# Performance work log

Measured on AMD Instinct MI355X. Metric: run time of the kernel, lower is better.

The kernel has to match this reference:

```python
import jax, jax.numpy as jnp
import numpy as np


def chamfer_l2(x, y):
    # x: [B,N1,3], y: [B,N2,3]; squared-L2 pairwise distances via Gram trick
    x2 = jnp.sum(x * x, axis=-1)                     # [B,N1]
    y2 = jnp.sum(y * y, axis=-1)                     # [B,N2]
    xy = jnp.einsum('bnd,bmd->bnm', x, y)            # [B,N1,N2]
    d = x2[:, :, None] + y2[:, None, :] - 2.0 * xy   # [B,N1,N2]
    cham_x = jnp.min(d, axis=2)                      # [B,N1] min over gt
    cham_y = jnp.min(d, axis=1)                      # [B,N2] min over pred
    return jnp.mean(cham_x) + jnp.mean(cham_y)


def setup_inputs() -> dict:
    key = jax.random.key(0)
    k1, k2, k3 = jax.random.split(key, 3)
    B = 4
    coarse_pc = jax.random.normal(k1, (B, 1024, 3), dtype=jnp.float32)
    fine_pc = jax.random.normal(k2, (B, 8192, 3), dtype=jnp.float32)
    gt_pc = jax.random.normal(k3, (B, 8192, 3), dtype=jnp.float32)
    return {"coarse_pc": coarse_pc, "fine_pc": fine_pc, "gt_pc": gt_pc,
            "param_coarse": 1000, "param_fine": 1000}


def reference(coarse_pc, fine_pc, gt_pc, param_coarse, param_fine):
    loss_coarse = chamfer_l2(coarse_pc, gt_pc) * param_coarse
    loss_fine = chamfer_l2(fine_pc, gt_pc) * param_fine
    return jnp.stack([loss_coarse, loss_fine])
```

## Files before the change

### kernel.cpp

```cpp
#include <hip/hip_runtime.h>

constexpr int NMINS = 102400;
constexpr int NBLK  = 2304;

typedef __attribute__((ext_vector_type(8)))  short bf16x8;
typedef __attribute__((ext_vector_type(16))) float f32x16;

__device__ __forceinline__ void split2(float v, unsigned& h, unsigned& l) {
    const unsigned uh = __float_as_uint(v) & 0xFFFF0000u;
    h = uh >> 16;
    l = __float_as_uint(v - __uint_as_float(uh)) >> 16;
}


__global__ __launch_bounds__(256, 3) void pccl_stage(
    const float* __restrict__ Xc, const float* __restrict__ Xf,
    const float* __restrict__ G, unsigned* __restrict__ mins,
    float* __restrict__ out)
{
    __shared__ uint4 alo[512];
    __shared__ uint4 ahi[512];
    const int tid  = threadIdx.x;
    const int lane = tid & 63;
    const int l31  = lane & 31;
    const bool hi  = lane >= 32;
    const int wv   = __builtin_amdgcn_readfirstlane(tid >> 6);
    const int W    = blockIdx.x;

    if (W == 0 && tid == 0) { out[0] = 0.0f; out[1] = 0.0f; }

    const float* Xp; const float* Yp;
    int NX, NY, ls, lc, local, mbase;
    if (W < 128)        { Xp=Xc; Yp=G;  NX=1024; NY=8192; ls=4; lc=1; local=W;      mbase=0; }
    else if (W < 256)   { Xp=G;  Yp=Xc; NX=8192; NY=1024; ls=1; lc=4; local=W-128;  mbase=4096; }
    else if (W < 1280)  { Xp=Xf; Yp=G;  NX=8192; NY=8192; ls=4; lc=4; local=W-256;  mbase=36864; }
    else                { Xp=G;  Yp=Xf; NX=8192; NY=8192; ls=4; lc=4; local=W-1280; mbase=69632; }
    const int split  = local & ((1 << ls) - 1);
    const int rest   = local >> ls;
    const int chunk4 = rest & ((1 << lc) - 1);
    const int b      = rest >> lc;

    const float* yg = Yp + ((size_t)b * NY + (size_t)split * 512) * 3;
    #pragma unroll
    for (int it = 0; it < 2; ++it) {
        const int pt = tid + 256 * it;
        const float y0 = yg[pt*3+0], y1 = yg[pt*3+1], y2 = yg[pt*3+2];
        const float w  = fmaf(y0, y0, fmaf(y1, y1, y2 * y2));
        unsigned h0, L0, h1, L1, h2, L2, hw, Lw;
        split2(y0, h0, L0); split2(y1, h1, L1);
        split2(y2, h2, L2); split2(w,  hw, Lw);
        alo[pt] = make_uint4(h0 | (L0 << 16), h0 | (h1 << 16),
                             L1 | (h1 << 16), h2 | (L2 << 16));
        ahi[pt] = make_uint4(h2 | (hw << 16), Lw, 0u, 0u);
    }

    const float* xg = Xp + ((size_t)b * NX + (size_t)chunk4 * 512 + (size_t)wv * 128) * 3;
    bf16x8 Bf[4]; float x2s[4];
    #pragma unroll
    for (int f = 0; f < 4; ++f) {
        const int p = f * 32 + l31;
        const float x0 = xg[p*3+0], x1 = xg[p*3+1], x2 = xg[p*3+2];
        x2s[f] = fmaf(x0, x0, fmaf(x1, x1, x2 * x2));
        unsigned sh0, sl0, sh1, sl1, sh2, sl2;
        split2(-2.f * x0, sh0, sl0);
        split2(-2.f * x1, sh1, sl1);
        split2(-2.f * x2, sh2, sl2);
        union { unsigned u[4]; bf16x8 v; } bu;
        bu.u[0] = hi ? (sl2 | (0x3F80u << 16)) : (sh0 | (sh0 << 16));
        bu.u[1] = hi ? 0x3F80u                 : (sl0 | (sh1 << 16));
        bu.u[2] = hi ? 0u                      : (sh1 | (sl1 << 16));
        bu.u[3] = hi ? 0u                      : (sh2 | (sh2 << 16));
        Bf[f] = bu.v;
    }

    float best[4][4];
    #pragma unroll
    for (int f = 0; f < 4; ++f)
        #pragma unroll
        for (int j = 0; j < 4; ++j) best[f][j] = 3.0e38f;

    const f32x16 zc = (f32x16)0.0f;
    const uint4* __restrict__ abase = hi ? ahi : alo;

    __syncthreads();

    #define FOLD(f, acc)                                                      \
        {                                                                     \
            _Pragma("unroll")                                                 \
            for (int j = 0; j < 4; ++j) {                                     \
                const float t3 = fminf(fminf((acc)[4*j], (acc)[4*j+1]),       \
                                       (acc)[4*j+2]);                         \
                best[f][j] = fminf(fminf(best[f][j], t3), (acc)[4*j+3]);      \
            }                                                                 \
        }

    uint4 dd = abase[l31];
    #pragma unroll 2
    for (int t = 0; t < 16; ++t) {
        union { uint4 u; bf16x8 v; } au; au.u = dd;
        const bf16x8 Af = au.v;
        const f32x16 a0 = __builtin_amdgcn_mfma_f32_32x32x16_bf16(Af, Bf[0], zc, 0, 0, 0);
        const f32x16 a1 = __builtin_amdgcn_mfma_f32_32x32x16_bf16(Af, Bf[1], zc, 0, 0, 0);
        const f32x16 a2 = __builtin_amdgcn_mfma_f32_32x32x16_bf16(Af, Bf[2], zc, 0, 0, 0);
        const f32x16 a3 = __builtin_amdgcn_mfma_f32_32x32x16_bf16(Af, Bf[3], zc, 0, 0, 0);
        dd = abase[(((t + 1) & 15) * 32) + l31];
        FOLD(0, a0);
        FOLD(1, a1);
        FOLD(2, a2);
        FOLD(3, a3);
    }
    #undef FOLD

    unsigned* mp = mins + mbase + b * NX + chunk4 * 512 + wv * 128;
    #pragma unroll
    for (int f = 0; f < 4; ++f) {
        float tm = fminf(fminf(best[f][0], best[f][1]),
                         fminf(best[f][2], best[f][3]));
        tm = fminf(tm, __shfl_xor(tm, 32, 64));
        const float d = fmaxf(x2s[f] + tm, 0.0f);
        atomicMin(mp + f * 32 + l31, __float_as_uint(d));
    }
}

__global__ __launch_bounds__(256) void pccl_sum(
    const unsigned* __restrict__ mins,
    const int* __restrict__ pc, const int* __restrict__ pf,
    float* __restrict__ out)
{
    const int tid  = threadIdx.x;
    const int lane = tid & 63;
    const int wv   = tid >> 6;
    const int q    = blockIdx.x * 256 + tid;
    const uint4 v  = ((const uint4*)mins)[q];
    float s = __uint_as_float(v.x) + __uint_as_float(v.y)
            + __uint_as_float(v.z) + __uint_as_float(v.w);
    #pragma unroll
    for (int off = 1; off < 64; off <<= 1) s += __shfl_xor(s, off, 64);
    __shared__ float sb[4];
    if (lane == 0) sb[wv] = s;
    __syncthreads();
    if (tid == 0) {
        const float t = sb[0] + sb[1] + sb[2] + sb[3];
        const int qb = blockIdx.x * 256;
        float w; int idx;
        if (qb < 1024)      { w = (1.f/4096.f)  * (float)pc[0]; idx = 0; }
        else if (qb < 9216) { w = (1.f/32768.f) * (float)pc[0]; idx = 0; }
        else                { w = (1.f/32768.f) * (float)pf[0]; idx = 1; }
        atomicAdd(out + idx, t * w);
    }
}

extern "C" void kernel_launch(void* const* d_in, const int* in_sizes, int n_in,
                              void* d_out, int out_size, void* d_ws, size_t ws_size,
                              hipStream_t stream) {
    const float* coarse = (const float*)d_in[0];
    const float* fine   = (const float*)d_in[1];
    const float* gt     = (const float*)d_in[2];
    const int*   pc     = (const int*)d_in[3];
    const int*   pf     = (const int*)d_in[4];
    float* out = (float*)d_out;
    unsigned* mins = (unsigned*)d_ws;

    pccl_stage<<<NBLK, 256, 0, stream>>>(coarse, fine, gt, mins, out);
    pccl_sum<<<100, 256, 0, stream>>>(mins, pc, pf, out);
}
```

Baseline: 81.99 us.

## Process three tiles per block with double-buffered LDS and prefetched loads

The grid shrinks to a third of its size, and each block now loops over three work tiles (block index plus multiples of the new grid size). While the MFMA loop runs on the current tile, the next tile's global loads are issued into registers. They are then packed into the other LDS buffer, and the previous tile's atomicMin stores are deferred so they overlap with later work. This hides global-load latency and per-block prologue cost. The price is higher register pressure under launch_bounds(256,3), double the LDS use, and fewer blocks to balance across CUs.

Measured after the change: 83.92 us. +2.4%, slower.

```diff
diff --git a/kernel.cpp b/kernel.cpp
--- a/kernel.cpp
+++ b/kernel.cpp
@@ -1,7 +1,7 @@
 #include <hip/hip_runtime.h>
 
 constexpr int NMINS = 102400;
-constexpr int NBLK  = 2304;
+constexpr int NBLK  = 768;
 
 typedef __attribute__((ext_vector_type(8)))  short bf16x8;
 typedef __attribute__((ext_vector_type(16))) float f32x16;
@@ -12,77 +12,89 @@
     l = __float_as_uint(v - __uint_as_float(uh)) >> 16;
 }
 
+__device__ __forceinline__ void packA(float y0, float y1, float y2,
+                                      uint4& lo, uint4& h4) {
+    const float w = fmaf(y0, y0, fmaf(y1, y1, y2 * y2));
+    unsigned h0, L0, h1, L1, h2, L2, hw, Lw;
+    split2(y0, h0, L0); split2(y1, h1, L1);
+    split2(y2, h2, L2); split2(w,  hw, Lw);
+    lo = make_uint4(h0 | (L0 << 16), h0 | (h1 << 16),
+                    L1 | (h1 << 16), h2 | (L2 << 16));
+    h4 = make_uint4(h2 | (hw << 16), Lw, 0u, 0u);
+}
+
+__device__ __forceinline__ bf16x8 packB(float x0, float x1, float x2, bool hi) {
+    unsigned sh0, sl0, sh1, sl1, sh2, sl2;
+    split2(-2.f * x0, sh0, sl0);
+    split2(-2.f * x1, sh1, sl1);
+    split2(-2.f * x2, sh2, sl2);
+    union { unsigned u[4]; bf16x8 v; } bu;
+    bu.u[0] = hi ? (sl2 | (0x3F80u << 16)) : (sh0 | (sh0 << 16));
+    bu.u[1] = hi ? 0x3F80u                 : (sl0 | (sh1 << 16));
+    bu.u[2] = hi ? 0u                      : (sh1 | (sl1 << 16));
+    bu.u[3] = hi ? 0u                      : (sh2 | (sh2 << 16));
+    return bu.v;
+}
+
+struct Geom { const float* Xp; const float* Yp; int NX, NY, mbase, split, chunk4, b; };
+
+__device__ __forceinline__ Geom decode(int W, const float* Xc,
+                                       const float* Xf, const float* G) {
+    Geom g; int ls, lc, local;
+    if (W < 128)        { g.Xp=Xc; g.Yp=G;  g.NX=1024; g.NY=8192; ls=4; lc=1; local=W;      g.mbase=0; }
+    else if (W < 256)   { g.Xp=G;  g.Yp=Xc; g.NX=8192; g.NY=1024; ls=1; lc=4; local=W-128;  g.mbase=4096; }
+    else if (W < 1280)  { g.Xp=Xf; g.Yp=G;  g.NX=8192; g.NY=8192; ls=4; lc=4; local=W-256;  g.mbase=36864; }
+    else                { g.Xp=G;  g.Yp=Xf; g.NX=8192; g.NY=8192; ls=4; lc=4; local=W-1280; g.mbase=69632; }
+    g.split  = local & ((1 << ls) - 1);
+    const int rest = local >> ls;
+    g.chunk4 = rest & ((1 << lc) - 1);
+    g.b      = rest >> lc;
+    return g;
+}
 
 __global__ __launch_bounds__(256, 3) void pccl_stage(
     const float* __restrict__ Xc, const float* __restrict__ Xf,
     const float* __restrict__ G, unsigned* __restrict__ mins,
     float* __restrict__ out)
 {
-    __shared__ uint4 alo[512];
-    __shared__ uint4 ahi[512];
+    __shared__ uint4 alo[2][512];
+    __shared__ uint4 ahi[2][512];
     const int tid  = threadIdx.x;
     const int lane = tid & 63;
     const int l31  = lane & 31;
     const bool hi  = lane >= 32;
     const int wv   = __builtin_amdgcn_readfirstlane(tid >> 6);
-    const int W    = blockIdx.x;
-
-    if (W == 0 && tid == 0) { out[0] = 0.0f; out[1] = 0.0f; }
-
-    const float* Xp; const float* Yp;
-    int NX, NY, ls, lc, local, mbase;
-    if (W < 128)        { Xp=Xc; Yp=G;  NX=1024; NY=8192; ls=4; lc=1; local=W;      mbase=0; }
-    else if (W < 256)   { Xp=G;  Yp=Xc; NX=8192; NY=1024; ls=1; lc=4; local=W-128;  mbase=4096; }
-    else if (W < 1280)  { Xp=Xf; Yp=G;  NX=8192; NY=8192; ls=4; lc=4; local=W-256;  mbase=36864; }
-    else                { Xp=G;  Yp=Xf; NX=8192; NY=8192; ls=4; lc=4; local=W-1280; mbase=69632; }
-    const int split  = local & ((1 << ls) - 1);
-    const int rest   = local >> ls;
-    const int chunk4 = rest & ((1 << lc) - 1);
-    const int b      = rest >> lc;
-
-    const float* yg = Yp + ((size_t)b * NY + (size_t)split * 512) * 3;
-    #pragma unroll
-    for (int it = 0; it < 2; ++it) {
-        const int pt = tid + 256 * it;
-        const float y0 = yg[pt*3+0], y1 = yg[pt*3+1], y2 = yg[pt*3+2];
-        const float w  = fmaf(y0, y0, fmaf(y1, y1, y2 * y2));
-        unsigned h0, L0, h1, L1, h2, L2, hw, Lw;
-        split2(y0, h0, L0); split2(y1, h1, L1);
-        split2(y2, h2, L2); split2(w,  hw, Lw);
-        alo[pt] = make_uint4(h0 | (L0 << 16), h0 | (h1 << 16),
-                             L1 | (h1 << 16), h2 | (L2 << 16));
-        ahi[pt] = make_uint4(h2 | (hw << 16), Lw, 0u, 0u);
-    }
-
-    const float* xg = Xp + ((size_t)b * NX + (size_t)chunk4 * 512 + (size_t)wv * 128) * 3;
+
+    if (blockIdx.x == 0 && tid == 0) { out[0] = 0.0f; out[1] = 0.0f; }
+
+    Geom g = decode(blockIdx.x, Xc, Xf, G);
+    {
+        const float* yg = g.Yp + ((size_t)g.b * g.NY + (size_t)g.split * 512) * 3;
+        #pragma unroll
+        for (int it = 0; it < 2; ++it) {
+            const int pt = tid + 256 * it;
+            uint4 lo, h4;
+            packA(yg[pt*3+0], yg[pt*3+1], yg[pt*3+2], lo, h4);
+            alo[0][pt] = lo; ahi[0][pt] = h4;
+        }
+    }
     bf16x8 Bf[4]; float x2s[4];
-    #pragma unroll
-    for (int f = 0; f < 4; ++f) {
-        const int p = f * 32 + l31;
-        const float x0 = xg[p*3+0], x1 = xg[p*3+1], x2 = xg[p*3+2];
-        x2s[f] = fmaf(x0, x0, fmaf(x1, x1, x2 * x2));
-        unsigned sh0, sl0, sh1, sl1, sh2, sl2;
-        split2(-2.f * x0, sh0, sl0);
-        split2(-2.f * x1, sh1, sl1);
-        split2(-2.f * x2, sh2, sl2);
-        union { unsigned u[4]; bf16x8 v; } bu;
-        bu.u[0] = hi ? (sl2 | (0x3F80u << 16)) : (sh0 | (sh0 << 16));
-        bu.u[1] = hi ? 0x3F80u                 : (sl0 | (sh1 << 16));
-        bu.u[2] = hi ? 0u                      : (sh1 | (sl1 << 16));
-        bu.u[3] = hi ? 0u                      : (sh2 | (sh2 << 16));
-        Bf[f] = bu.v;
-    }
-
-    float best[4][4];
-    #pragma unroll
-    for (int f = 0; f < 4; ++f)
-        #pragma unroll
-        for (int j = 0; j < 4; ++j) best[f][j] = 3.0e38f;
-
+    {
+        const float* xg = g.Xp + ((size_t)g.b * g.NX + (size_t)g.chunk4 * 512
+                                  + (size_t)wv * 128) * 3;
+        #pragma unroll
+        for (int f = 0; f < 4; ++f) {
+            const int p = f * 32 + l31;
+            const float x0 = xg[p*3+0], x1 = xg[p*3+1], x2 = xg[p*3+2];
+            x2s[f] = fmaf(x0, x0, fmaf(x1, x1, x2 * x2));
+            Bf[f] = packB(x0, x1, x2, hi);
+        }
+    }
     const f32x16 zc = (f32x16)0.0f;
-    const uint4* __restrict__ abase = hi ? ahi : alo;
-
     __syncthreads();
+
+    unsigned* mpp = nullptr;
+    float d4[4];
 
     #define FOLD(f, acc)                                                      \
         {                                                                     \
@@ -94,32 +106,95 @@
             }                                                                 \
         }
 
-    uint4 dd = abase[l31];
-    #pragma unroll 2
-    for (int t = 0; t < 16; ++t) {
-        union { uint4 u; bf16x8 v; } au; au.u = dd;
-        const bf16x8 Af = au.v;
-        const f32x16 a0 = __builtin_amdgcn_mfma_f32_32x32x16_bf16(Af, Bf[0], zc, 0, 0, 0);
-        const f32x16 a1 = __builtin_amdgcn_mfma_f32_32x32x16_bf16(Af, Bf[1], zc, 0, 0, 0);
-        const f32x16 a2 = __builtin_amdgcn_mfma_f32_32x32x16_bf16(Af, Bf[2], zc, 0, 0, 0);
-        const f32x16 a3 = __builtin_amdgcn_mfma_f32_32x32x16_bf16(Af, Bf[3], zc, 0, 0, 0);
-        dd = abase[(((t + 1) & 15) * 32) + l31];
-        FOLD(0, a0);
-        FOLD(1, a1);
-        FOLD(2, a2);
-        FOLD(3, a3);
+    #pragma unroll
+    for (int c = 0; c < 3; ++c) {
+        const int cb = c & 1;
+
+        if (c > 0) {
+            #pragma unroll
+            for (int f = 0; f < 4; ++f)
+                atomicMin(mpp + f * 32 + l31, __float_as_uint(d4[f]));
+        }
+
+        float yn[6]; float xn[12]; Geom gn;
+        if (c < 2) {
+            gn = decode(blockIdx.x + NBLK * (c + 1), Xc, Xf, G);
+            const float* yg = gn.Yp + ((size_t)gn.b * gn.NY
+                                       + (size_t)gn.split * 512) * 3;
+            #pragma unroll
+            for (int it = 0; it < 2; ++it) {
+                const int pt = tid + 256 * it;
+                yn[it*3+0] = yg[pt*3+0];
+                yn[it*3+1] = yg[pt*3+1];
+                yn[it*3+2] = yg[pt*3+2];
+            }
+            const float* xg = gn.Xp + ((size_t)gn.b * gn.NX
+                                       + (size_t)gn.chunk4 * 512
+                                       + (size_t)wv * 128) * 3;
+            #pragma unroll
+            for (int f = 0; f < 4; ++f) {
+                const int p = f * 32 + l31;
+                xn[f*3+0] = xg[p*3+0];
+                xn[f*3+1] = xg[p*3+1];
+                xn[f*3+2] = xg[p*3+2];
+            }
+        }
+
+        float best[4][4];
+        #pragma unroll
+        for (int f = 0; f < 4; ++f)
+            #pragma unroll
+            for (int j = 0; j < 4; ++j) best[f][j] = 3.0e38f;
+
+        const uint4* __restrict__ abase = hi ? ahi[cb] : alo[cb];
+        uint4 dd = abase[l31];
+        #pragma unroll 2
+        for (int t = 0; t < 16; ++t) {
+            union { uint4 u; bf16x8 v; } au; au.u = dd;
+            const bf16x8 Af = au.v;
+            const f32x16 a0 = __builtin_amdgcn_mfma_f32_32x32x16_bf16(Af, Bf[0], zc, 0, 0, 0);
+            const f32x16 a1 = __builtin_amdgcn_mfma_f32_32x32x16_bf16(Af, Bf[1], zc, 0, 0, 0);
+            const f32x16 a2 = __builtin_amdgcn_mfma_f32_32x32x16_bf16(Af, Bf[2], zc, 0, 0, 0);
+            const f32x16 a3 = __builtin_amdgcn_mfma_f32_32x32x16_bf16(Af, Bf[3], zc, 0, 0, 0);
+            dd = abase[(((t + 1) & 15) * 32) + l31];
+            FOLD(0, a0);
+            FOLD(1, a1);
+            FOLD(2, a2);
+            FOLD(3, a3);
+        }
+
+        mpp = mins + g.mbase + g.b * g.NX + g.chunk4 * 512 + wv * 128;
+        #pragma unroll
+        for (int f = 0; f < 4; ++f) {
+            float tm = fminf(fminf(best[f][0], best[f][1]),
+                             fminf(best[f][2], best[f][3]));
+            tm = fminf(tm, __shfl_xor(tm, 32, 64));
+            d4[f] = fmaxf(x2s[f] + tm, 0.0f);
+        }
+
+        if (c < 2) {
+            #pragma unroll
+            for (int it = 0; it < 2; ++it) {
+                const int pt = tid + 256 * it;
+                uint4 lo, h4;
+                packA(yn[it*3+0], yn[it*3+1], yn[it*3+2], lo, h4);
+                alo[cb ^ 1][pt] = lo; ahi[cb ^ 1][pt] = h4;
+            }
+            #pragma unroll
+            for (int f = 0; f < 4; ++f) {
+                const float x0 = xn[f*3+0], x1 = xn[f*3+1], x2 = xn[f*3+2];
+                x2s[f] = fmaf(x0, x0, fmaf(x1, x1, x2 * x2));
+                Bf[f] = packB(x0, x1, x2, hi);
+            }
+            g = gn;
+            __syncthreads();
+        }
     }
     #undef FOLD
 
-    unsigned* mp = mins + mbase + b * NX + chunk4 * 512 + wv * 128;
     #pragma unroll
-    for (int f = 0; f < 4; ++f) {
-        float tm = fminf(fminf(best[f][0], best[f][1]),
-                         fminf(best[f][2], best[f][3]));
-        tm = fminf(tm, __shfl_xor(tm, 32, 64));
-        const float d = fmaxf(x2s[f] + tm, 0.0f);
-        atomicMin(mp + f * 32 + l31, __float_as_uint(d));
-    }
+    for (int f = 0; f < 4; ++f)
+        atomicMin(mpp + f * 32 + l31, __float_as_uint(d4[f]));
 }
 
 __global__ __launch_bounds__(256) void pccl_sum(
```
